# Optimization experiments

Measured on AMD Instinct MI355X. Metric: run time of the kernel, lower is better.

## Reference

```python
import jax, jax.numpy as jnp
import numpy as np


def setup_inputs() -> dict:
    key = jax.random.key(0)
    ks = jax.random.split(key, 6)
    bs, n_src, n_tgt = 4, 4096, 16384
    c_src, c_tgt = 256, 128
    xyz_target = jax.random.uniform(ks[0], (bs, n_tgt, 3), dtype=jnp.float32)
    xyz_source = jax.random.uniform(ks[1], (bs, n_src, 3), dtype=jnp.float32)
    feats_target = jax.random.normal(ks[2], (bs, n_tgt, c_tgt), dtype=jnp.float32)
    feats_source = jax.random.normal(ks[3], (bs, n_src, c_src), dtype=jnp.float32)
    # SharedMlP 1x1 conv weights (1,1,cin,cout) squeezed to (cin,cout)
    w1 = jax.random.normal(ks[4], (c_src + c_tgt, 256), dtype=jnp.float32) * (1.0 / np.sqrt(c_src + c_tgt))
    w2 = jax.random.normal(ks[5], (256, 256), dtype=jnp.float32) * (1.0 / np.sqrt(256))
    return {"xyz_target": xyz_target, "xyz_source": xyz_source,
            "feats_target": feats_target, "feats_source": feats_source,
            "w1": w1, "w2": w2}


def reference(xyz_target, xyz_source, feats_target, feats_source, w1, w2):
    # --- three_nn: full pairwise euclidean distance [bs, n_tgt, n_src] ---
    diff = xyz_target[:, :, None, :] - xyz_source[:, None, :, :]
    dis = jnp.linalg.norm(diff, axis=-1)                      # bs, n_tgt, n_src
    neg_dis, idx = jax.lax.top_k(-dis, 3)                     # 3 nearest
    nn_dis = jnp.maximum(-neg_dis, 1e-10)                     # bs, n_tgt, 3
    inv = 1.0 / nn_dis
    weight = inv / jnp.sum(inv, axis=-1, keepdims=True)       # bs, n_tgt, 3
    # --- three_interpolate: batched gather + weighted reduce ---
    feats_sel = jax.vmap(lambda f, i: f[i])(feats_source, idx)  # bs, n_tgt, 3, c
    w_sum = jnp.sum(weight, axis=-1, keepdims=True) + 1e-6
    interp = jnp.einsum('btk,btkc->btc', weight, feats_sel) / w_sum
    # --- concat skip features, 1x1-conv MLP (pointwise matmul) ---
    x = jnp.concatenate([interp, feats_target], axis=2)       # bs, n_tgt, 384
    x = jax.nn.relu(jnp.einsum('btc,cd->btd', x, w1))
    x = jax.nn.relu(jnp.einsum('btc,cd->btd', x, w2))
    return x
```

## Files before the change

kernel.cpp:

```cpp
#include <hip/hip_runtime.h>
#include <hip/hip_bf16.h>
#include <stdint.h>

#define BS 4
#define NS 4096
#define NT 16384
#define CT 128
#define NOUT 256
#define MTOT (BS*NT)
#define GR 8
#define NC (GR*GR*GR)
#define HCELL 0.125f

typedef __attribute__((ext_vector_type(4))) float floatx4;
typedef __attribute__((ext_vector_type(8))) unsigned short ushortx8;
typedef __attribute__((ext_vector_type(8))) __bf16 bf16x8;

__device__ __forceinline__ unsigned short f2bf(float f) {
  unsigned int u = __builtin_bit_cast(unsigned int, f);
  u += 0x7FFFu + ((u >> 16) & 1u);
  return (unsigned short)(u >> 16);
}
__device__ __forceinline__ float bf2f(unsigned short u) {
  return __builtin_bit_cast(float, ((unsigned int)u) << 16);
}
__device__ __forceinline__ int cell_of(float x) {
  int c = (int)(x * 8.0f);
  return min(7, max(0, c));
}
__device__ __forceinline__ bf16x8 ldb16(const unsigned short* p) {
  return __builtin_bit_cast(bf16x8, *(const ushortx8*)p);
}
__device__ __forceinline__ ushortx8 wsum8(ushortx8 a, ushortx8 c, ushortx8 e,
                                          float w0, float w1v, float w2v) {
  ushortx8 o;
  #pragma unroll
  for (int q = 0; q < 8; ++q)
    o[q] = f2bf(w0*bf2f(a[q]) + w1v*bf2f(c[q]) + w2v*bf2f(e[q]));
  return o;
}

__global__ __launch_bounds__(1024) void prep_kernel(
    const float* __restrict__ xyzs, const float* __restrict__ xyzt,
    const float* __restrict__ w1, const float* __restrict__ w2,
    float4* __restrict__ bsrc, int* __restrict__ soff, float4* __restrict__ stgt,
    unsigned short* __restrict__ w1at, unsigned short* __restrict__ w1bt,
    unsigned short* __restrict__ w2t) {
  int bid = blockIdx.x, tid = threadIdx.x;
  if (bid < 8) {
    __shared__ int cnt[NC];
    __shared__ int scan[NC];
    int b = bid & 3;
    bool isrc = bid < 4;
    int per = isrc ? (NS >> 10) : (NT >> 10);
    const float* in = isrc ? xyzs + (size_t)b * NS * 3 : xyzt + (size_t)b * NT * 3;
    float4* outp = isrc ? bsrc + (size_t)b * NS : stgt + (size_t)b * NT;
    if (tid < NC) cnt[tid] = 0;
    __syncthreads();
    for (int k = 0; k < per; ++k) {
      int p = k * 1024 + tid;
      float x = in[3*p], y = in[3*p+1], z = in[3*p+2];
      int c = (cell_of(z) * GR + cell_of(y)) * GR + cell_of(x);
      atomicAdd(&cnt[c], 1);
    }
    __syncthreads();
    if (tid < NC) scan[tid] = cnt[tid];
    __syncthreads();
    for (int off = 1; off < NC; off <<= 1) {
      int v = (tid < NC && tid >= off) ? scan[tid - off] : 0;
      __syncthreads();
      if (tid < NC) scan[tid] += v;
      __syncthreads();
    }
    if (tid < NC) {
      int excl = scan[tid] - cnt[tid];
      cnt[tid] = excl;
      if (isrc) soff[b * (NC + 1) + tid] = excl;
    }
    if (isrc && tid == 0) soff[b * (NC + 1) + NC] = NS;
    __syncthreads();
    for (int k = 0; k < per; ++k) {
      int p = k * 1024 + tid;
      float x = in[3*p], y = in[3*p+1], z = in[3*p+2];
      int c = (cell_of(z) * GR + cell_of(y)) * GR + cell_of(x);
      int slot = atomicAdd(&cnt[c], 1);
      outp[slot] = make_float4(x, y, z, __int_as_float(p));
    }
  } else {
    int i = (bid - 8) * 1024 + tid;
    int n = i >> 8, k = i & 255;
    w1at[i] = f2bf(w1[k * NOUT + n]);
    w2t[i]  = f2bf(w2[k * NOUT + n]);
    if (i < 256 * 128) {
      int n2 = i >> 7, k2 = i & 127;
      w1bt[i] = f2bf(w1[(256 + k2) * NOUT + n2]);
    }
  }
}

__device__ __forceinline__ void ins3(float sc, int jj,
    float& d0, float& d1, float& d2, int& i0, int& i1, int& i2) {
  bool l0 = sc < d0, l1 = sc < d1, l2 = sc < d2;
  d2 = l1 ? d1 : (l2 ? sc : d2);
  i2 = l1 ? i1 : (l2 ? jj : i2);
  d1 = l0 ? d0 : (l1 ? sc : d1);
  i1 = l0 ? i0 : (l1 ? jj : i1);
  d0 = l0 ? sc : d0;
  i0 = l0 ? jj : i0;
}

__device__ __forceinline__ void pair_merge(float& d0, float& d1, float& d2,
                                           int& i0, int& i1, int& i2,
                                           int delta, int sub) {
  float e0 = __shfl_xor(d0, delta);
  float e1 = __shfl_xor(d1, delta);
  float e2 = __shfl_xor(d2, delta);
  int   y0 = __shfl_xor(i0, delta);
  int   y1 = __shfl_xor(i1, delta);
  int   y2 = __shfl_xor(i2, delta);
  float a0,a1,a2,b0,b1,b2; int x0,x1,x2,z0,z1,z2;
  if ((sub & delta) == 0) { a0=d0;a1=d1;a2=d2; x0=i0;x1=i1;x2=i2;
                            b0=e0;b1=e1;b2=e2; z0=y0;z1=y1;z2=y2; }
  else                    { a0=e0;a1=e1;a2=e2; x0=y0;x1=y1;x2=y2;
                            b0=d0;b1=d1;b2=d2; z0=i0;z1=i1;z2=i2; }
  bool t = a0 <= b0;
  d0 = t ? a0 : b0; i0 = t ? x0 : z0;
  float na0 = t ? a1 : a0; int nx0 = t ? x1 : x0;
  float na1 = t ? a2 : a1; int nx1 = t ? x2 : x1;
  float nb0 = t ? b0 : b1; int nz0 = t ? z0 : z1;
  float nb1 = t ? b1 : b2; int nz1 = t ? z1 : z2;
  t = na0 <= nb0;
  d1 = t ? na0 : nb0; i1 = t ? nx0 : nz0;
  float ma0 = t ? na1 : na0; int mx0 = t ? nx1 : nx0;
  float mb0 = t ? nb0 : nb1; int mz0 = t ? nz0 : nz1;
  t = ma0 <= mb0;
  d2 = t ? ma0 : mb0; i2 = t ? mx0 : mz0;
}

__global__ __launch_bounds__(256) void nn_kernel(const float4* __restrict__ stgt,
    const float4* __restrict__ bsrc, const int* __restrict__ soff,
    int* __restrict__ idx_out, float* __restrict__ w_out) {
  __shared__ float4 s_src[NS];
  __shared__ int s_off[NC + 1];
  __shared__ float4 s_badq[128];
  __shared__ int s_badn;
  int tid = threadIdx.x;
  int b = blockIdx.x >> 7;
  int tseg = blockIdx.x & 127;
  if (tid == 0) s_badn = 0;
  for (int i = tid; i < NS; i += 256) s_src[i] = bsrc[(size_t)b * NS + i];
  for (int i = tid; i < NC + 1; i += 256) s_off[i] = soff[b * (NC + 1) + i];
  __syncthreads();
  int tpair = tid >> 1, half = tid & 1;
  float4 tg = stgt[(size_t)b * NT + tseg * 128 + tpair];
  float tx = tg.x, ty = tg.y, tz = tg.z;
  int cx = cell_of(tx), cy = cell_of(ty), cz = cell_of(tz);
  int wx = min(max(cx, 1), 6) - 1;
  int wy = min(max(cy, 1), 6) - 1;
  int wz = min(max(cz, 1), 6) - 1;
  float d0 = 1e30f, d1 = 1e30f, d2 = 1e30f;
  int i0 = 0, i1 = 0, i2 = 0;
  for (int r = half; r < 9; r += 2) {
    int ez = wz + r / 3, ey = wy + r % 3;
    int rowc = (ez * GR + ey) * GR + wx;
    int lo = s_off[rowc], hi = s_off[rowc + 3];
    for (int p = lo; p < hi; ++p) {
      float4 s = s_src[p];
      float dx = tx - s.x, dy = ty - s.y, dz = tz - s.z;
      float q = dx*dx + dy*dy + dz*dz;
      ins3(q, __float_as_int(s.w), d0, d1, d2, i0, i1, i2);
    }
  }
  pair_merge(d0, d1, d2, i0, i1, i2, 1, half);
  float clx = fminf(wx > 0 ? tx - wx * HCELL : 1e30f,
                    wx + 3 < GR ? (wx + 3) * HCELL - tx : 1e30f);
  float cly = fminf(wy > 0 ? ty - wy * HCELL : 1e30f,
                    wy + 3 < GR ? (wy + 3) * HCELL - ty : 1e30f);
  float clz = fminf(wz > 0 ? tz - wz * HCELL : 1e30f,
                    wz + 3 < GR ? (wz + 3) * HCELL - tz : 1e30f);
  float cl = fminf(clx, fminf(cly, clz));
  bool bad = d2 > cl * cl;
  if (half == 0) {
    if (bad) {
      int slot = atomicAdd(&s_badn, 1);
      s_badq[slot] = make_float4(tx, ty, tz, __int_as_float(tseg * 128 + tpair));
    } else {
      float r0 = fmaxf(sqrtf(d0), 1e-10f);
      float r1 = fmaxf(sqrtf(d1), 1e-10f);
      float r2 = fmaxf(sqrtf(d2), 1e-10f);
      float v0 = 1.f/r0, v1 = 1.f/r1, v2 = 1.f/r2;
      float sc = 1.f / ((v0 + v1 + v2) * (1.f + 1e-6f));
      size_t o = ((size_t)b * NT + tseg * 128 + tpair) * 3;
      idx_out[o] = i0; idx_out[o+1] = i1; idx_out[o+2] = i2;
      w_out[o] = v0*sc; w_out[o+1] = v1*sc; w_out[o+2] = v2*sc;
    }
  }
  __syncthreads();
  int nbad = s_badn;
  int wv = tid >> 6, ln = tid & 63;
  for (int e = wv; e < nbad; e += 4) {
    float4 tq = s_badq[e];
    float qx = tq.x, qy = tq.y, qz = tq.z;
    float f0 = 1e30f, f1 = 1e30f, f2 = 1e30f;
    int   j0 = 0, j1 = 0, j2 = 0;
    for (int p = ln; p < NS; p += 64) {
      float4 s = s_src[p];
      float dx = qx - s.x, dy = qy - s.y, dz = qz - s.z;
      float q = dx*dx + dy*dy + dz*dz;
      ins3(q, __float_as_int(s.w), f0, f1, f2, j0, j1, j2);
    }
    #pragma unroll
    for (int delta = 1; delta <= 32; delta <<= 1)
      pair_merge(f0, f1, f2, j0, j1, j2, delta, ln);
    if (ln == 0) {
      float r0 = fmaxf(sqrtf(f0), 1e-10f);
      float r1 = fmaxf(sqrtf(f1), 1e-10f);
      float r2 = fmaxf(sqrtf(f2), 1e-10f);
      float v0 = 1.f/r0, v1 = 1.f/r1, v2 = 1.f/r2;
      float sc = 1.f / ((v0 + v1 + v2) * (1.f + 1e-6f));
      size_t o = ((size_t)b * NT + __float_as_int(tq.w)) * 3;
      idx_out[o] = j0; idx_out[o+1] = j1; idx_out[o+2] = j2;
      w_out[o] = v0*sc; w_out[o+1] = v1*sc; w_out[o+2] = v2*sc;
    }
  }
}

__global__ __launch_bounds__(256, 4) void gemm_g(const float* __restrict__ fs,
    const unsigned short* __restrict__ w1at, unsigned short* __restrict__ G) {
  constexpr int LDT = 264;
  __shared__ __attribute__((aligned(16))) unsigned short sA[32 * LDT];
  int tid = threadIdx.x;
  int m0 = blockIdx.x * 32;
  int wave = tid >> 6, lane = tid & 63;
  int wn = wave * 64;
  int fr = lane & 15, quad = lane >> 4;
  const unsigned short* wbase = w1at + (size_t)(wn + fr) * 256 + quad * 8;
  #pragma unroll
  for (int i = 0; i < 4; ++i) {
    int u = tid + 256 * i;
    int r = u >> 5, k8 = (u & 31) * 8;
    const float* src = fs + (size_t)(m0 + r) * 256 + k8;
    float4 f0 = *(const float4*)src;
    float4 f1 = *(const float4*)(src + 4);
    ushortx8 o;
    o[0]=f2bf(f0.x); o[1]=f2bf(f0.y); o[2]=f2bf(f0.z); o[3]=f2bf(f0.w);
    o[4]=f2bf(f1.x); o[5]=f2bf(f1.y); o[6]=f2bf(f1.z); o[7]=f2bf(f1.w);
    *(ushortx8*)&sA[r * LDT + k8] = o;
  }
  __syncthreads();
  floatx4 zero = {0.f, 0.f, 0.f, 0.f};
  floatx4 acc[2][4];
  #pragma unroll
  for (int i = 0; i < 2; ++i)
    #pragma unroll
    for (int j = 0; j < 4; ++j) acc[i][j] = zero;
  bf16x8 wb[3][4];
  #pragma unroll
  for (int ni = 0; ni < 4; ++ni) wb[0][ni] = ldb16(wbase + (size_t)ni*16*256 + 0*32);
  #pragma unroll
  for (int ni = 0; ni < 4; ++ni) wb[1][ni] = ldb16(wbase + (size_t)ni*16*256 + 1*32);
  __builtin_amdgcn_sched_barrier(0);
  #pragma unroll
  for (int kt = 0; kt < 8; ++kt) {
    if (kt < 6) {
      #pragma unroll
      for (int ni = 0; ni < 4; ++ni)
        wb[(kt+2)%3][ni] = ldb16(wbase + (size_t)ni*16*256 + (kt+2)*32);
    }
    __builtin_amdgcn_sched_barrier(0);
    bf16x8 af[2];
    #pragma unroll
    for (int mi = 0; mi < 2; ++mi)
      af[mi] = ldb16(&sA[(mi*16 + fr)*LDT + kt*32 + quad*8]);
    #pragma unroll
    for (int mi = 0; mi < 2; ++mi)
      #pragma unroll
      for (int ni = 0; ni < 4; ++ni)
        acc[mi][ni] = __builtin_amdgcn_mfma_f32_16x16x32_bf16(
            af[mi], wb[kt%3][ni], acc[mi][ni], 0, 0, 0);
  }
  #pragma unroll
  for (int mi = 0; mi < 2; ++mi)
    #pragma unroll
    for (int ni = 0; ni < 4; ++ni)
      #pragma unroll
      for (int r = 0; r < 4; ++r) {
        int grow = m0 + mi*16 + quad*4 + r;
        int gcol = wn + ni*16 + fr;
        G[(size_t)grow * 256 + gcol] = f2bf(acc[mi][ni][r]);
      }
}

__global__ __launch_bounds__(512, 4) void fused_mlp(const float* __restrict__ ft,
    const unsigned short* __restrict__ G, const int* __restrict__ idxb,
    const float* __restrict__ wgtb, const float4* __restrict__ stgt,
    const unsigned short* __restrict__ w1bt, const unsigned short* __restrict__ w2t,
    float* __restrict__ out) {
  constexpr int LDI = 264;
  constexpr int LDF = 136;
  __shared__ __attribute__((aligned(16))) unsigned short sI[64 * LDI];
  __shared__ __attribute__((aligned(16))) unsigned short sF[64 * LDF];
  int tid = threadIdx.x;
  int row0 = blockIdx.x * 64;
  int b = row0 >> 14;
  const float4* st = stgt + ((size_t)b << 14) + (row0 & (NT - 1));
  const float* ftb = ft + (size_t)b * NT * CT;
  float* outb = out + (size_t)b * NT * NOUT;
  int wave = tid >> 6, lane = tid & 63;
  int wn = wave * 32;
  int fr = lane & 15, quad = lane >> 4;

  int r = tid >> 3, seg = tid & 7;
  const int* ip = idxb + (size_t)(row0 + r) * 3;
  const float* wp = wgtb + (size_t)(row0 + r) * 3;
  int g0i = ip[0], g1i = ip[1], g2i = ip[2];
  float w0 = wp[0], w1v = wp[1], w2v = wp[2];
  int rA = tid >> 4;
  int rB = rA + 32;
  int orig0 = __float_as_int(st[rA].w);
  int orig1 = __float_as_int(st[rB].w);

  bf16x8 wb1[2][4];
  #pragma unroll
  for (int ni = 0; ni < 2; ++ni)
    #pragma unroll
    for (int kt = 0; kt < 4; ++kt)
      wb1[ni][kt] = ldb16(w1bt + (size_t)(wn + ni*16 + fr) * CT + kt*32 + quad*8);
  __builtin_amdgcn_sched_barrier(0);

  const unsigned short* Gb = G + ((size_t)b << 20);
  const unsigned short* g0 = Gb + ((size_t)g0i << 8) + seg * 32;
  const unsigned short* g1 = Gb + ((size_t)g1i << 8) + seg * 32;
  const unsigned short* g2 = Gb + ((size_t)g2i << 8) + seg * 32;
  ushortx8 a0 = *(const ushortx8*)(g0 + 0);
  ushortx8 a1 = *(const ushortx8*)(g0 + 8);
  ushortx8 a2 = *(const ushortx8*)(g0 + 16);
  ushortx8 a3 = *(const ushortx8*)(g0 + 24);
  ushortx8 c0 = *(const ushortx8*)(g1 + 0);
  ushortx8 c1 = *(const ushortx8*)(g1 + 8);
  ushortx8 c2 = *(const ushortx8*)(g1 + 16);
  ushortx8 c3 = *(const ushortx8*)(g1 + 24);
  ushortx8 e0 = *(const ushortx8*)(g2 + 0);
  ushortx8 e1 = *(const ushortx8*)(g2 + 8);
  ushortx8 e2 = *(const ushortx8*)(g2 + 16);
  ushortx8 e3 = *(const ushortx8*)(g2 + 24);

  int k8 = (tid & 15) * 8;
  const float* srcA = ftb + (size_t)orig0 * CT + k8;
  const float* srcB = ftb + (size_t)orig1 * CT + k8;
  float4 fa0 = *(const float4*)srcA;
  float4 fa1 = *(const float4*)(srcA + 4);
  float4 fb0 = *(const float4*)srcB;
  float4 fb1 = *(const float4*)(srcB + 4);
  __builtin_amdgcn_sched_barrier(0);

  {
    unsigned short* dst = &sI[r * LDI + seg * 32];
    *(ushortx8*)(dst + 0)  = wsum8(a0, c0, e0, w0, w1v, w2v);
    *(ushortx8*)(dst + 8)  = wsum8(a1, c1, e1, w0, w1v, w2v);
    *(ushortx8*)(dst + 16) = wsum8(a2, c2, e2, w0, w1v, w2v);
    *(ushortx8*)(dst + 24) = wsum8(a3, c3, e3, w0, w1v, w2v);
  }
  {
    ushortx8 o;
    o[0]=f2bf(fa0.x); o[1]=f2bf(fa0.y); o[2]=f2bf(fa0.z); o[3]=f2bf(fa0.w);
    o[4]=f2bf(fa1.x); o[5]=f2bf(fa1.y); o[6]=f2bf(fa1.z); o[7]=f2bf(fa1.w);
    *(ushortx8*)&sF[rA * LDF + k8] = o;
    ushortx8 p;
    p[0]=f2bf(fb0.x); p[1]=f2bf(fb0.y); p[2]=f2bf(fb0.z); p[3]=f2bf(fb0.w);
    p[4]=f2bf(fb1.x); p[5]=f2bf(fb1.y); p[6]=f2bf(fb1.z); p[7]=f2bf(fb1.w);
    *(ushortx8*)&sF[rB * LDF + k8] = p;
  }
  __syncthreads();

  floatx4 zero = {0.f, 0.f, 0.f, 0.f};
  floatx4 acc[4][2];
  #pragma unroll
  for (int i = 0; i < 4; ++i)
    #pragma unroll
    for (int j = 0; j < 2; ++j) acc[i][j] = zero;

  #pragma unroll
  for (int kt = 0; kt < 4; ++kt) {
    bf16x8 af[4];
    #pragma unroll
    for (int mi = 0; mi < 4; ++mi)
      af[mi] = ldb16(&sF[(mi*16 + fr)*LDF + kt*32 + quad*8]);
    #pragma unroll
    for (int mi = 0; mi < 4; ++mi)
      #pragma unroll
      for (int ni = 0; ni < 2; ++ni)
        acc[mi][ni] = __builtin_amdgcn_mfma_f32_16x16x32_bf16(
            af[mi], wb1[ni][kt], acc[mi][ni], 0, 0, 0);
  }

  bf16x8 wb2[2][8];
  #pragma unroll
  for (int ni = 0; ni < 2; ++ni)
    #pragma unroll
    for (int kt = 0; kt < 8; ++kt)
      wb2[ni][kt] = ldb16(w2t + (size_t)(wn + ni*16 + fr) * NOUT + kt*32 + quad*8);
  __builtin_amdgcn_sched_barrier(0);

  #pragma unroll
  for (int mi = 0; mi < 4; ++mi)
    #pragma unroll
    for (int ni = 0; ni < 2; ++ni)
      #pragma unroll
      for (int rr = 0; rr < 4; ++rr) {
        int lr = mi*16 + quad*4 + rr;
        int lc = wn + ni*16 + fr;
        float v = acc[mi][ni][rr] + bf2f(sI[lr * LDI + lc]);
        sI[lr * LDI + lc] = f2bf(fmaxf(v, 0.f));
      }
  __syncthreads();

  #pragma unroll
  for (int i = 0; i < 4; ++i)
    #pragma unroll
    for (int j = 0; j < 2; ++j) acc[i][j] = zero;
  #pragma unroll
  for (int kt = 0; kt < 8; ++kt) {
    bf16x8 af[4];
    #pragma unroll
    for (int mi = 0; mi < 4; ++mi)
      af[mi] = ldb16(&sI[(mi*16 + fr)*LDI + kt*32 + quad*8]);
    #pragma unroll
    for (int mi = 0; mi < 4; ++mi)
      #pragma unroll
      for (int ni = 0; ni < 2; ++ni)
        acc[mi][ni] = __builtin_amdgcn_mfma_f32_16x16x32_bf16(
            af[mi], wb2[ni][kt], acc[mi][ni], 0, 0, 0);
  }
  #pragma unroll
  for (int mi = 0; mi < 4; ++mi)
    #pragma unroll
    for (int rr = 0; rr < 4; ++rr) {
      int lr = mi*16 + quad*4 + rr;
      int orig = __float_as_int(st[lr].w);
      float* orow = outb + (size_t)orig * NOUT;
      #pragma unroll
      for (int ni = 0; ni < 2; ++ni)
        orow[wn + ni*16 + fr] = fmaxf(acc[mi][ni][rr], 0.f);
    }
}

extern "C" void kernel_launch(void* const* d_in, const int* in_sizes, int n_in,
                              void* d_out, int out_size, void* d_ws, size_t ws_size,
                              hipStream_t stream) {
  (void)in_sizes; (void)n_in; (void)out_size; (void)ws_size;
  const float* xyzt = (const float*)d_in[0];
  const float* xyzs = (const float*)d_in[1];
  const float* ft   = (const float*)d_in[2];
  const float* fs   = (const float*)d_in[3];
  const float* w1   = (const float*)d_in[4];
  const float* w2   = (const float*)d_in[5];

  char* p = (char*)d_ws;
  unsigned short* w1at = (unsigned short*)p; p += (size_t)256*256*2;
  unsigned short* w1bt = (unsigned short*)p; p += (size_t)256*128*2;
  unsigned short* w2t  = (unsigned short*)p; p += (size_t)256*256*2;
  int*   idxb = (int*)p;   p += (size_t)MTOT*3*4;
  float* wgtb = (float*)p; p += (size_t)MTOT*3*4;
  unsigned short* G = (unsigned short*)p; p += (size_t)BS*NS*NOUT*2;
  float4* bsrc = (float4*)p; p += (size_t)BS*NS*16;
  float4* stgt = (float4*)p; p += (size_t)BS*NT*16;
  int*    soff = (int*)p;

  hipLaunchKernelGGL(prep_kernel, dim3(8 + 64), dim3(1024), 0, stream,
                     xyzs, xyzt, w1, w2, bsrc, soff, stgt, w1at, w1bt, w2t);
  hipLaunchKernelGGL(nn_kernel, dim3(512), dim3(256), 0, stream, stgt, bsrc, soff, idxb, wgtb);
  hipLaunchKernelGGL(gemm_g, dim3(BS*NS/32), dim3(256), 0, stream, fs, w1at, G);
  hipLaunchKernelGGL(fused_mlp, dim3(MTOT/64), dim3(512), 0, stream,
                     ft, G, idxb, wgtb, stgt, w1bt, w2t, (float*)d_out);
}
```

Before: 192.4 us.

## Merge NN search and source GEMM into one launch, read sources from global

Combines the nearest-neighbour kernel and the source-feature GEMM into a single launch where block ranges pick the role, so the two independent stages can run at the same time and one launch is removed. The NN part now gives each target four threads instead of two, uses half as many targets per block, and reads sorted source points straight from global/L2 instead of staging all 4096 into 64KB of LDS, which lowers LDS use and raises occupancy. The grid-cell prefix scan in prep is rewritten as a wave-shuffle scan with fewer barriers. The risk is that global-memory reads in the brute-force fallback path are slower than LDS, and the bad-query buffer is smaller (64 entries).

New measurement: 197.8 us. 2.8% more time.

```diff
diff --git a/kernel.cpp b/kernel.cpp
--- a/kernel.cpp
+++ b/kernel.cpp
@@ -49,7 +49,7 @@
   int bid = blockIdx.x, tid = threadIdx.x;
   if (bid < 8) {
     __shared__ int cnt[NC];
-    __shared__ int scan[NC];
+    __shared__ int wtot[16];
     int b = bid & 3;
     bool isrc = bid < 4;
     int per = isrc ? (NS >> 10) : (NT >> 10);
@@ -64,16 +64,28 @@
       atomicAdd(&cnt[c], 1);
     }
     __syncthreads();
-    if (tid < NC) scan[tid] = cnt[tid];
-    __syncthreads();
-    for (int off = 1; off < NC; off <<= 1) {
-      int v = (tid < NC && tid >= off) ? scan[tid - off] : 0;
-      __syncthreads();
-      if (tid < NC) scan[tid] += v;
-      __syncthreads();
-    }
+    int l = tid & 63, w = tid >> 6;
+    int v = (tid < NC) ? cnt[tid] : 0;
+    #pragma unroll
+    for (int d = 1; d < 64; d <<= 1) {
+      int t = __shfl_up(v, d);
+      if (l >= d) v += t;
+    }
+    if (l == 63 && w < 8) wtot[w] = v;
+    __syncthreads();
+    if (w == 0 && l < 8) {
+      int s = wtot[l];
+      #pragma unroll
+      for (int d = 1; d < 8; d <<= 1) {
+        int t = __shfl_up(s, d);
+        if (l >= d) s += t;
+      }
+      wtot[l] = s;
+    }
+    __syncthreads();
     if (tid < NC) {
-      int excl = scan[tid] - cnt[tid];
+      int incl = v + (w > 0 ? wtot[w-1] : 0);
+      int excl = incl - cnt[tid];
       cnt[tid] = excl;
       if (isrc) soff[b * (NC + 1) + tid] = excl;
     }
@@ -137,158 +149,159 @@
   d2 = t ? ma0 : mb0; i2 = t ? mx0 : mz0;
 }
 
-__global__ __launch_bounds__(256) void nn_kernel(const float4* __restrict__ stgt,
-    const float4* __restrict__ bsrc, const int* __restrict__ soff,
-    int* __restrict__ idx_out, float* __restrict__ w_out) {
-  __shared__ float4 s_src[NS];
-  __shared__ int s_off[NC + 1];
-  __shared__ float4 s_badq[128];
-  __shared__ int s_badn;
+__global__ __launch_bounds__(256, 4) void nng_kernel(
+    const float4* __restrict__ stgt, const float4* __restrict__ bsrc,
+    const int* __restrict__ soff, int* __restrict__ idx_out,
+    float* __restrict__ w_out, const float* __restrict__ fs,
+    const unsigned short* __restrict__ w1at, unsigned short* __restrict__ G) {
+  __shared__ __attribute__((aligned(16))) char smem[16896];
   int tid = threadIdx.x;
-  int b = blockIdx.x >> 7;
-  int tseg = blockIdx.x & 127;
-  if (tid == 0) s_badn = 0;
-  for (int i = tid; i < NS; i += 256) s_src[i] = bsrc[(size_t)b * NS + i];
-  for (int i = tid; i < NC + 1; i += 256) s_off[i] = soff[b * (NC + 1) + i];
-  __syncthreads();
-  int tpair = tid >> 1, half = tid & 1;
-  float4 tg = stgt[(size_t)b * NT + tseg * 128 + tpair];
-  float tx = tg.x, ty = tg.y, tz = tg.z;
-  int cx = cell_of(tx), cy = cell_of(ty), cz = cell_of(tz);
-  int wx = min(max(cx, 1), 6) - 1;
-  int wy = min(max(cy, 1), 6) - 1;
-  int wz = min(max(cz, 1), 6) - 1;
-  float d0 = 1e30f, d1 = 1e30f, d2 = 1e30f;
-  int i0 = 0, i1 = 0, i2 = 0;
-  for (int r = half; r < 9; r += 2) {
-    int ez = wz + r / 3, ey = wy + r % 3;
-    int rowc = (ez * GR + ey) * GR + wx;
-    int lo = s_off[rowc], hi = s_off[rowc + 3];
-    for (int p = lo; p < hi; ++p) {
-      float4 s = s_src[p];
-      float dx = tx - s.x, dy = ty - s.y, dz = tz - s.z;
-      float q = dx*dx + dy*dy + dz*dz;
-      ins3(q, __float_as_int(s.w), d0, d1, d2, i0, i1, i2);
-    }
-  }
-  pair_merge(d0, d1, d2, i0, i1, i2, 1, half);
-  float clx = fminf(wx > 0 ? tx - wx * HCELL : 1e30f,
-                    wx + 3 < GR ? (wx + 3) * HCELL - tx : 1e30f);
-  float cly = fminf(wy > 0 ? ty - wy * HCELL : 1e30f,
-                    wy + 3 < GR ? (wy + 3) * HCELL - ty : 1e30f);
-  float clz = fminf(wz > 0 ? tz - wz * HCELL : 1e30f,
-                    wz + 3 < GR ? (wz + 3) * HCELL - tz : 1e30f);
-  float cl = fminf(clx, fminf(cly, clz));
-  bool bad = d2 > cl * cl;
-  if (half == 0) {
-    if (bad) {
-      int slot = atomicAdd(&s_badn, 1);
-      s_badq[slot] = make_float4(tx, ty, tz, __int_as_float(tseg * 128 + tpair));
-    } else {
-      float r0 = fmaxf(sqrtf(d0), 1e-10f);
-      float r1 = fmaxf(sqrtf(d1), 1e-10f);
-      float r2 = fmaxf(sqrtf(d2), 1e-10f);
-      float v0 = 1.f/r0, v1 = 1.f/r1, v2 = 1.f/r2;
-      float sc = 1.f / ((v0 + v1 + v2) * (1.f + 1e-6f));
-      size_t o = ((size_t)b * NT + tseg * 128 + tpair) * 3;
-      idx_out[o] = i0; idx_out[o+1] = i1; idx_out[o+2] = i2;
-      w_out[o] = v0*sc; w_out[o+1] = v1*sc; w_out[o+2] = v2*sc;
-    }
-  }
-  __syncthreads();
-  int nbad = s_badn;
-  int wv = tid >> 6, ln = tid & 63;
-  for (int e = wv; e < nbad; e += 4) {
-    float4 tq = s_badq[e];
-    float qx = tq.x, qy = tq.y, qz = tq.z;
-    float f0 = 1e30f, f1 = 1e30f, f2 = 1e30f;
-    int   j0 = 0, j1 = 0, j2 = 0;
-    for (int p = ln; p < NS; p += 64) {
-      float4 s = s_src[p];
-      float dx = qx - s.x, dy = qy - s.y, dz = qz - s.z;
-      float q = dx*dx + dy*dy + dz*dz;
-      ins3(q, __float_as_int(s.w), f0, f1, f2, j0, j1, j2);
-    }
-    #pragma unroll
-    for (int delta = 1; delta <= 32; delta <<= 1)
-      pair_merge(f0, f1, f2, j0, j1, j2, delta, ln);
-    if (ln == 0) {
-      float r0 = fmaxf(sqrtf(f0), 1e-10f);
-      float r1 = fmaxf(sqrtf(f1), 1e-10f);
-      float r2 = fmaxf(sqrtf(f2), 1e-10f);
-      float v0 = 1.f/r0, v1 = 1.f/r1, v2 = 1.f/r2;
-      float sc = 1.f / ((v0 + v1 + v2) * (1.f + 1e-6f));
-      size_t o = ((size_t)b * NT + __float_as_int(tq.w)) * 3;
-      idx_out[o] = j0; idx_out[o+1] = j1; idx_out[o+2] = j2;
-      w_out[o] = v0*sc; w_out[o+1] = v1*sc; w_out[o+2] = v2*sc;
-    }
-  }
-}
-
-__global__ __launch_bounds__(256, 4) void gemm_g(const float* __restrict__ fs,
-    const unsigned short* __restrict__ w1at, unsigned short* __restrict__ G) {
-  constexpr int LDT = 264;
-  __shared__ __attribute__((aligned(16))) unsigned short sA[32 * LDT];
-  int tid = threadIdx.x;
-  int m0 = blockIdx.x * 32;
-  int wave = tid >> 6, lane = tid & 63;
-  int wn = wave * 64;
-  int fr = lane & 15, quad = lane >> 4;
-  const unsigned short* wbase = w1at + (size_t)(wn + fr) * 256 + quad * 8;
-  #pragma unroll
-  for (int i = 0; i < 4; ++i) {
-    int u = tid + 256 * i;
-    int r = u >> 5, k8 = (u & 31) * 8;
-    const float* src = fs + (size_t)(m0 + r) * 256 + k8;
-    float4 f0 = *(const float4*)src;
-    float4 f1 = *(const float4*)(src + 4);
-    ushortx8 o;
-    o[0]=f2bf(f0.x); o[1]=f2bf(f0.y); o[2]=f2bf(f0.z); o[3]=f2bf(f0.w);
-    o[4]=f2bf(f1.x); o[5]=f2bf(f1.y); o[6]=f2bf(f1.z); o[7]=f2bf(f1.w);
-    *(ushortx8*)&sA[r * LDT + k8] = o;
-  }
-  __syncthreads();
-  floatx4 zero = {0.f, 0.f, 0.f, 0.f};
-  floatx4 acc[2][4];
-  #pragma unroll
-  for (int i = 0; i < 2; ++i)
-    #pragma unroll
-    for (int j = 0; j < 4; ++j) acc[i][j] = zero;
-  bf16x8 wb[3][4];
-  #pragma unroll
-  for (int ni = 0; ni < 4; ++ni) wb[0][ni] = ldb16(wbase + (size_t)ni*16*256 + 0*32);
-  #pragma unroll
-  for (int ni = 0; ni < 4; ++ni) wb[1][ni] = ldb16(wbase + (size_t)ni*16*256 + 1*32);
-  __builtin_amdgcn_sched_barrier(0);
-  #pragma unroll
-  for (int kt = 0; kt < 8; ++kt) {
-    if (kt < 6) {
+  if (blockIdx.x < 1024) {
+    int* s_off = (int*)smem;
+    float4* s_badq = (float4*)(smem + 2064);
+    int* s_badn = (int*)(smem + 2064 + 64 * 16);
+    int b = blockIdx.x >> 8;
+    int tseg = blockIdx.x & 255;
+    if (tid == 0) *s_badn = 0;
+    for (int i = tid; i < NC + 1; i += 256) s_off[i] = soff[b * (NC + 1) + i];
+    __syncthreads();
+    const float4* src = bsrc + (size_t)b * NS;
+    int t4 = tid >> 2, h = tid & 3;
+    float4 tg = stgt[(size_t)b * NT + tseg * 64 + t4];
+    float tx = tg.x, ty = tg.y, tz = tg.z;
+    int cx = cell_of(tx), cy = cell_of(ty), cz = cell_of(tz);
+    int wx = min(max(cx, 1), 6) - 1;
+    int wy = min(max(cy, 1), 6) - 1;
+    int wz = min(max(cz, 1), 6) - 1;
+    float d0 = 1e30f, d1 = 1e30f, d2 = 1e30f;
+    int i0 = 0, i1 = 0, i2 = 0;
+    for (int r = h; r < 9; r += 4) {
+      int ez = wz + r / 3, ey = wy + r % 3;
+      int rowc = (ez * GR + ey) * GR + wx;
+      int lo = s_off[rowc], hi = s_off[rowc + 3];
+      for (int p = lo; p < hi; ++p) {
+        float4 s = src[p];
+        float dx = tx - s.x, dy = ty - s.y, dz = tz - s.z;
+        float q = dx*dx + dy*dy + dz*dz;
+        ins3(q, __float_as_int(s.w), d0, d1, d2, i0, i1, i2);
+      }
+    }
+    pair_merge(d0, d1, d2, i0, i1, i2, 1, h);
+    pair_merge(d0, d1, d2, i0, i1, i2, 2, h);
+    float clx = fminf(wx > 0 ? tx - wx * HCELL : 1e30f,
+                      wx + 3 < GR ? (wx + 3) * HCELL - tx : 1e30f);
+    float cly = fminf(wy > 0 ? ty - wy * HCELL : 1e30f,
+                      wy + 3 < GR ? (wy + 3) * HCELL - ty : 1e30f);
+    float clz = fminf(wz > 0 ? tz - wz * HCELL : 1e30f,
+                      wz + 3 < GR ? (wz + 3) * HCELL - tz : 1e30f);
+    float cl = fminf(clx, fminf(cly, clz));
+    bool bad = d2 > cl * cl;
+    if (h == 0) {
+      if (bad) {
+        int slot = atomicAdd(s_badn, 1);
+        s_badq[slot] = make_float4(tx, ty, tz, __int_as_float(tseg * 64 + t4));
+      } else {
+        float r0 = fmaxf(sqrtf(d0), 1e-10f);
+        float r1 = fmaxf(sqrtf(d1), 1e-10f);
+        float r2 = fmaxf(sqrtf(d2), 1e-10f);
+        float v0 = 1.f/r0, v1 = 1.f/r1, v2 = 1.f/r2;
+        float sc = 1.f / ((v0 + v1 + v2) * (1.f + 1e-6f));
+        size_t o = ((size_t)b * NT + tseg * 64 + t4) * 3;
+        idx_out[o] = i0; idx_out[o+1] = i1; idx_out[o+2] = i2;
+        w_out[o] = v0*sc; w_out[o+1] = v1*sc; w_out[o+2] = v2*sc;
+      }
+    }
+    __syncthreads();
+    int nbad = *s_badn;
+    int wv = tid >> 6, ln = tid & 63;
+    for (int e = wv; e < nbad; e += 4) {
+      float4 tq = s_badq[e];
+      float qx = tq.x, qy = tq.y, qz = tq.z;
+      float f0 = 1e30f, f1 = 1e30f, f2 = 1e30f;
+      int   j0 = 0, j1 = 0, j2 = 0;
+      for (int p = ln; p < NS; p += 64) {
+        float4 s = src[p];
+        float dx = qx - s.x, dy = qy - s.y, dz = qz - s.z;
+        float q = dx*dx + dy*dy + dz*dz;
+        ins3(q, __float_as_int(s.w), f0, f1, f2, j0, j1, j2);
+      }
+      #pragma unroll
+      for (int delta = 1; delta <= 32; delta <<= 1)
+        pair_merge(f0, f1, f2, j0, j1, j2, delta, ln);
+      if (ln == 0) {
+        float r0 = fmaxf(sqrtf(f0), 1e-10f);
+        float r1 = fmaxf(sqrtf(f1), 1e-10f);
+        float r2 = fmaxf(sqrtf(f2), 1e-10f);
+        float v0 = 1.f/r0, v1 = 1.f/r1, v2 = 1.f/r2;
+        float sc = 1.f / ((v0 + v1 + v2) * (1.f + 1e-6f));
+        size_t o = ((size_t)b * NT + __float_as_int(tq.w)) * 3;
+        idx_out[o] = j0; idx_out[o+1] = j1; idx_out[o+2] = j2;
+        w_out[o] = v0*sc; w_out[o+1] = v1*sc; w_out[o+2] = v2*sc;
+      }
+    }
+  } else {
+    constexpr int LDT = 264;
+    unsigned short* sA = (unsigned short*)smem;
+    int m0 = (blockIdx.x - 1024) * 32;
+    int wave = tid >> 6, lane = tid & 63;
+    int wn = wave * 64;
+    int fr = lane & 15, quad = lane >> 4;
+    const unsigned short* wbase = w1at + (size_t)(wn + fr) * 256 + quad * 8;
+    #pragma unroll
+    for (int i = 0; i < 4; ++i) {
+      int u = tid + 256 * i;
+      int r = u >> 5, k8 = (u & 31) * 8;
+      const float* src = fs + (size_t)(m0 + r) * 256 + k8;
+      float4 f0 = *(const float4*)src;
+      float4 f1 = *(const float4*)(src + 4);
+      ushortx8 o;
+      o[0]=f2bf(f0.x); o[1]=f2bf(f0.y); o[2]=f2bf(f0.z); o[3]=f2bf(f0.w);
+      o[4]=f2bf(f1.x); o[5]=f2bf(f1.y); o[6]=f2bf(f1.z); o[7]=f2bf(f1.w);
+      *(ushortx8*)&sA[r * LDT + k8] = o;
+    }
+    __syncthreads();
+    floatx4 zero = {0.f, 0.f, 0.f, 0.f};
+    floatx4 acc[2][4];
+    #pragma unroll
+    for (int i = 0; i < 2; ++i)
+      #pragma unroll
+      for (int j = 0; j < 4; ++j) acc[i][j] = zero;
+    bf16x8 wb[3][4];
+    #pragma unroll
+    for (int ni = 0; ni < 4; ++ni) wb[0][ni] = ldb16(wbase + (size_t)ni*16*256 + 0*32);
+    #pragma unroll
+    for (int ni = 0; ni < 4; ++ni) wb[1][ni] = ldb16(wbase + (size_t)ni*16*256 + 1*32);
+    __builtin_amdgcn_sched_barrier(0);
+    #pragma unroll
+    for (int kt = 0; kt < 8; ++kt) {
+      if (kt < 6) {
+        #pragma unroll
+        for (int ni = 0; ni < 4; ++ni)
+          wb[(kt+2)%3][ni] = ldb16(wbase + (size_t)ni*16*256 + (kt+2)*32);
+      }
+      __builtin_amdgcn_sched_barrier(0);
+      bf16x8 af[2];
+      #pragma unroll
+      for (int mi = 0; mi < 2; ++mi)
+        af[mi] = ldb16(&sA[(mi*16 + fr)*LDT + kt*32 + quad*8]);
+      #pragma unroll
+      for (int mi = 0; mi < 2; ++mi)
+        #pragma unroll
+        for (int ni = 0; ni < 4; ++ni)
+          acc[mi][ni] = __builtin_amdgcn_mfma_f32_16x16x32_bf16(
+              af[mi], wb[kt%3][ni], acc[mi][ni], 0, 0, 0);
+    }
+    #pragma unroll
+    for (int mi = 0; mi < 2; ++mi)
       #pragma unroll
       for (int ni = 0; ni < 4; ++ni)
-        wb[(kt+2)%3][ni] = ldb16(wbase + (size_t)ni*16*256 + (kt+2)*32);
-    }
-    __builtin_amdgcn_sched_barrier(0);
-    bf16x8 af[2];
-    #pragma unroll
-    for (int mi = 0; mi < 2; ++mi)
-      af[mi] = ldb16(&sA[(mi*16 + fr)*LDT + kt*32 + quad*8]);
-    #pragma unroll
-    for (int mi = 0; mi < 2; ++mi)
-      #pragma unroll
-      for (int ni = 0; ni < 4; ++ni)
-        acc[mi][ni] = __builtin_amdgcn_mfma_f32_16x16x32_bf16(
-            af[mi], wb[kt%3][ni], acc[mi][ni], 0, 0, 0);
-  }
-  #pragma unroll
-  for (int mi = 0; mi < 2; ++mi)
-    #pragma unroll
-    for (int ni = 0; ni < 4; ++ni)
-      #pragma unroll
-      for (int r = 0; r < 4; ++r) {
-        int grow = m0 + mi*16 + quad*4 + r;
-        int gcol = wn + ni*16 + fr;
-        G[(size_t)grow * 256 + gcol] = f2bf(acc[mi][ni][r]);
-      }
+        #pragma unroll
+        for (int r = 0; r < 4; ++r) {
+          int grow = m0 + mi*16 + quad*4 + r;
+          int gcol = wn + ni*16 + fr;
+          G[(size_t)grow * 256 + gcol] = f2bf(acc[mi][ni][r]);
+        }
+  }
 }
 
 __global__ __launch_bounds__(512, 4) void fused_mlp(const float* __restrict__ ft,
@@ -469,8 +482,8 @@
 
   hipLaunchKernelGGL(prep_kernel, dim3(8 + 64), dim3(1024), 0, stream,
                      xyzs, xyzt, w1, w2, bsrc, soff, stgt, w1at, w1bt, w2t);
-  hipLaunchKernelGGL(nn_kernel, dim3(512), dim3(256), 0, stream, stgt, bsrc, soff, idxb, wgtb);
-  hipLaunchKernelGGL(gemm_g, dim3(BS*NS/32), dim3(256), 0, stream, fs, w1at, G);
+  hipLaunchKernelGGL(nng_kernel, dim3(1024 + 512), dim3(256), 0, stream,
+                     stgt, bsrc, soff, idxb, wgtb, fs, w1at, G);
   hipLaunchKernelGGL(fused_mlp, dim3(MTOT/64), dim3(512), 0, stream,
                      ft, G, idxb, wgtb, stgt, w1bt, w2t, (float*)d_out);
 }
```

## Hand-schedule global loads with inline asm and use wave-shuffle scan in prep

Applied to the files above, without the earlier changes.

Replaces the compiler-scheduled gather, skip-feature and weight loads in the MLP kernel with inline-asm global_load_dwordx4 and explicit s_waitcnt points. The W1 and W2 fragment loads are issued later so they overlap the interpolation and ReLU/LDS stages, and they are awaited only before their MFMA loops, which should hide weight-load latency. Separately, the prep kernel's LDS Hillis-Steele scan with many barriers is replaced by a wave-level shuffle scan plus a small cross-wave fix-up. The inline asm bypasses the compiler's own hazard and wait tracking, which adds correctness risk and may raise register pressure.

New measurement: 189.9 us (median of 2 runs). No clear change (-1.3%).

```diff
diff --git a/kernel.cpp b/kernel.cpp
--- a/kernel.cpp
+++ b/kernel.cpp
@@ -40,6 +40,10 @@
   return o;
 }
 
+#define GLD16(dst, ptr, off) \
+  asm volatile("global_load_dwordx4 %0, %1, off offset:" #off \
+               : "=&v"(dst) : "v"(ptr))
+
 __global__ __launch_bounds__(1024) void prep_kernel(
     const float* __restrict__ xyzs, const float* __restrict__ xyzt,
     const float* __restrict__ w1, const float* __restrict__ w2,
@@ -49,7 +53,7 @@
   int bid = blockIdx.x, tid = threadIdx.x;
   if (bid < 8) {
     __shared__ int cnt[NC];
-    __shared__ int scan[NC];
+    __shared__ int wtot[16];
     int b = bid & 3;
     bool isrc = bid < 4;
     int per = isrc ? (NS >> 10) : (NT >> 10);
@@ -64,16 +68,28 @@
       atomicAdd(&cnt[c], 1);
     }
     __syncthreads();
-    if (tid < NC) scan[tid] = cnt[tid];
+    int l = tid & 63, w = tid >> 6;
+    int v = (tid < NC) ? cnt[tid] : 0;
+    #pragma unroll
+    for (int d = 1; d < 64; d <<= 1) {
+      int t = __shfl_up(v, d);
+      if (l >= d) v += t;
+    }
+    if (l == 63 && w < 8) wtot[w] = v;
     __syncthreads();
-    for (int off = 1; off < NC; off <<= 1) {
-      int v = (tid < NC && tid >= off) ? scan[tid - off] : 0;
-      __syncthreads();
-      if (tid < NC) scan[tid] += v;
-      __syncthreads();
-    }
+    if (w == 0 && l < 8) {
+      int s = wtot[l];
+      #pragma unroll
+      for (int d = 1; d < 8; d <<= 1) {
+        int t = __shfl_up(s, d);
+        if (l >= d) s += t;
+      }
+      wtot[l] = s;
+    }
+    __syncthreads();
     if (tid < NC) {
-      int excl = scan[tid] - cnt[tid];
+      int incl = v + (w > 0 ? wtot[w-1] : 0);
+      int excl = incl - cnt[tid];
       cnt[tid] = excl;
       if (isrc) soff[b * (NC + 1) + tid] = excl;
     }
@@ -320,39 +336,36 @@
   int orig0 = __float_as_int(st[rA].w);
   int orig1 = __float_as_int(st[rB].w);
 
-  bf16x8 wb1[2][4];
-  #pragma unroll
-  for (int ni = 0; ni < 2; ++ni)
-    #pragma unroll
-    for (int kt = 0; kt < 4; ++kt)
-      wb1[ni][kt] = ldb16(w1bt + (size_t)(wn + ni*16 + fr) * CT + kt*32 + quad*8);
-  __builtin_amdgcn_sched_barrier(0);
-
   const unsigned short* Gb = G + ((size_t)b << 20);
   const unsigned short* g0 = Gb + ((size_t)g0i << 8) + seg * 32;
   const unsigned short* g1 = Gb + ((size_t)g1i << 8) + seg * 32;
   const unsigned short* g2 = Gb + ((size_t)g2i << 8) + seg * 32;
-  ushortx8 a0 = *(const ushortx8*)(g0 + 0);
-  ushortx8 a1 = *(const ushortx8*)(g0 + 8);
-  ushortx8 a2 = *(const ushortx8*)(g0 + 16);
-  ushortx8 a3 = *(const ushortx8*)(g0 + 24);
-  ushortx8 c0 = *(const ushortx8*)(g1 + 0);
-  ushortx8 c1 = *(const ushortx8*)(g1 + 8);
-  ushortx8 c2 = *(const ushortx8*)(g1 + 16);
-  ushortx8 c3 = *(const ushortx8*)(g1 + 24);
-  ushortx8 e0 = *(const ushortx8*)(g2 + 0);
-  ushortx8 e1 = *(const ushortx8*)(g2 + 8);
-  ushortx8 e2 = *(const ushortx8*)(g2 + 16);
-  ushortx8 e3 = *(const ushortx8*)(g2 + 24);
-
   int k8 = (tid & 15) * 8;
   const float* srcA = ftb + (size_t)orig0 * CT + k8;
   const float* srcB = ftb + (size_t)orig1 * CT + k8;
-  float4 fa0 = *(const float4*)srcA;
-  float4 fa1 = *(const float4*)(srcA + 4);
-  float4 fb0 = *(const float4*)srcB;
-  float4 fb1 = *(const float4*)(srcB + 4);
+
+  ushortx8 a0, a1, a2, a3, c0, c1, c2, c3, e0, e1, e2, e3;
+  GLD16(a0, g0, 0);  GLD16(a1, g0, 16);  GLD16(a2, g0, 32);  GLD16(a3, g0, 48);
+  GLD16(c0, g1, 0);  GLD16(c1, g1, 16);  GLD16(c2, g1, 32);  GLD16(c3, g1, 48);
+  GLD16(e0, g2, 0);  GLD16(e1, g2, 16);  GLD16(e2, g2, 32);  GLD16(e3, g2, 48);
+  floatx4 fa0, fa1, fb0, fb1;
+  GLD16(fa0, srcA, 0);  GLD16(fa1, srcA, 16);
+  GLD16(fb0, srcB, 0);  GLD16(fb1, srcB, 16);
+
+  asm volatile("s_waitcnt vmcnt(0)"
+               : "+v"(a0), "+v"(a1), "+v"(a2), "+v"(a3),
+                 "+v"(c0), "+v"(c1), "+v"(c2), "+v"(c3),
+                 "+v"(e0), "+v"(e1), "+v"(e2), "+v"(e3),
+                 "+v"(fa0), "+v"(fa1), "+v"(fb0), "+v"(fb1));
   __builtin_amdgcn_sched_barrier(0);
+
+  const unsigned short* w1p0 = w1bt + (size_t)(wn + fr) * CT + quad * 8;
+  const unsigned short* w1p1 = w1bt + (size_t)(wn + 16 + fr) * CT + quad * 8;
+  bf16x8 wb1[2][4];
+  GLD16(wb1[0][0], w1p0, 0);   GLD16(wb1[0][1], w1p0, 64);
+  GLD16(wb1[0][2], w1p0, 128); GLD16(wb1[0][3], w1p0, 192);
+  GLD16(wb1[1][0], w1p1, 0);   GLD16(wb1[1][1], w1p1, 64);
+  GLD16(wb1[1][2], w1p1, 128); GLD16(wb1[1][3], w1p1, 192);
 
   {
     unsigned short* dst = &sI[r * LDI + seg * 32];
@@ -363,15 +376,20 @@
   }
   {
     ushortx8 o;
-    o[0]=f2bf(fa0.x); o[1]=f2bf(fa0.y); o[2]=f2bf(fa0.z); o[3]=f2bf(fa0.w);
-    o[4]=f2bf(fa1.x); o[5]=f2bf(fa1.y); o[6]=f2bf(fa1.z); o[7]=f2bf(fa1.w);
+    o[0]=f2bf(fa0[0]); o[1]=f2bf(fa0[1]); o[2]=f2bf(fa0[2]); o[3]=f2bf(fa0[3]);
+    o[4]=f2bf(fa1[0]); o[5]=f2bf(fa1[1]); o[6]=f2bf(fa1[2]); o[7]=f2bf(fa1[3]);
     *(ushortx8*)&sF[rA * LDF + k8] = o;
     ushortx8 p;
-    p[0]=f2bf(fb0.x); p[1]=f2bf(fb0.y); p[2]=f2bf(fb0.z); p[3]=f2bf(fb0.w);
-    p[4]=f2bf(fb1.x); p[5]=f2bf(fb1.y); p[6]=f2bf(fb1.z); p[7]=f2bf(fb1.w);
+    p[0]=f2bf(fb0[0]); p[1]=f2bf(fb0[1]); p[2]=f2bf(fb0[2]); p[3]=f2bf(fb0[3]);
+    p[4]=f2bf(fb1[0]); p[5]=f2bf(fb1[1]); p[6]=f2bf(fb1[2]); p[7]=f2bf(fb1[3]);
     *(ushortx8*)&sF[rB * LDF + k8] = p;
   }
   __syncthreads();
+
+  asm volatile("s_waitcnt vmcnt(0)"
+               : "+v"(wb1[0][0]), "+v"(wb1[0][1]), "+v"(wb1[0][2]), "+v"(wb1[0][3]),
+                 "+v"(wb1[1][0]), "+v"(wb1[1][1]), "+v"(wb1[1][2]), "+v"(wb1[1][3]));
+  __builtin_amdgcn_sched_barrier(0);
 
   floatx4 zero = {0.f, 0.f, 0.f, 0.f};
   floatx4 acc[4][2];
@@ -394,13 +412,17 @@
             af[mi], wb1[ni][kt], acc[mi][ni], 0, 0, 0);
   }
 
+  const unsigned short* w2p0 = w2t + (size_t)(wn + fr) * NOUT + quad * 8;
+  const unsigned short* w2p1 = w2t + (size_t)(wn + 16 + fr) * NOUT + quad * 8;
   bf16x8 wb2[2][8];
-  #pragma unroll
-  for (int ni = 0; ni < 2; ++ni)
-    #pragma unroll
-    for (int kt = 0; kt < 8; ++kt)
-      wb2[ni][kt] = ldb16(w2t + (size_t)(wn + ni*16 + fr) * NOUT + kt*32 + quad*8);
-  __builtin_amdgcn_sched_barrier(0);
+  GLD16(wb2[0][0], w2p0, 0);   GLD16(wb2[0][1], w2p0, 64);
+  GLD16(wb2[0][2], w2p0, 128); GLD16(wb2[0][3], w2p0, 192);
+  GLD16(wb2[0][4], w2p0, 256); GLD16(wb2[0][5], w2p0, 320);
+  GLD16(wb2[0][6], w2p0, 384); GLD16(wb2[0][7], w2p0, 448);
+  GLD16(wb2[1][0], w2p1, 0);   GLD16(wb2[1][1], w2p1, 64);
+  GLD16(wb2[1][2], w2p1, 128); GLD16(wb2[1][3], w2p1, 192);
+  GLD16(wb2[1][4], w2p1, 256); GLD16(wb2[1][5], w2p1, 320);
+  GLD16(wb2[1][6], w2p1, 384); GLD16(wb2[1][7], w2p1, 448);
 
   #pragma unroll
   for (int mi = 0; mi < 4; ++mi)
@@ -414,6 +436,13 @@
         sI[lr * LDI + lc] = f2bf(fmaxf(v, 0.f));
       }
   __syncthreads();
+
+  asm volatile("s_waitcnt vmcnt(0)"
+               : "+v"(wb2[0][0]), "+v"(wb2[0][1]), "+v"(wb2[0][2]), "+v"(wb2[0][3]),
+                 "+v"(wb2[0][4]), "+v"(wb2[0][5]), "+v"(wb2[0][6]), "+v"(wb2[0][7]),
+                 "+v"(wb2[1][0]), "+v"(wb2[1][1]), "+v"(wb2[1][2]), "+v"(wb2[1][3]),
+                 "+v"(wb2[1][4]), "+v"(wb2[1][5]), "+v"(wb2[1][6]), "+v"(wb2[1][7]));
+  __builtin_amdgcn_sched_barrier(0);
 
   #pragma unroll
   for (int i = 0; i < 4; ++i)
```
